# Optimization experiments

Hardware: AMD Instinct MI355X
Metric: run time of the kernel (lower is better)

The kernel has to match this reference:

```python
import jax, jax.numpy as jnp
import numpy as np

B, N, D, H = 8, 2048, 256, 4
HD = D // H


def setup_inputs() -> dict:
    key = jax.random.key(0)
    ks = jax.random.split(key, 12)
    s = 1.0 / np.sqrt(D)
    inp = {
        "node_features": jax.random.normal(ks[0], (B, N, D), dtype=jnp.float32),
        "causal_mask": jnp.tril(jnp.ones((N, N), dtype=jnp.float32)),
        "Wq": jax.random.normal(ks[1], (D, D), dtype=jnp.float32) * s,
        "bq": jnp.zeros((D,), dtype=jnp.float32),
        "Wk": jax.random.normal(ks[2], (D, D), dtype=jnp.float32) * s,
        "bk": jnp.zeros((D,), dtype=jnp.float32),
        "Wv": jax.random.normal(ks[3], (D, D), dtype=jnp.float32) * s,
        "bv": jnp.zeros((D,), dtype=jnp.float32),
        "Wo": jax.random.normal(ks[4], (D, D), dtype=jnp.float32) * s,
        "bo": jnp.zeros((D,), dtype=jnp.float32),
        "Wu": jax.random.normal(ks[5], (2 * D, D), dtype=jnp.float32) * (1.0 / np.sqrt(2 * D)),
        "bu": jnp.zeros((D,), dtype=jnp.float32),
    }
    return inp


def reference(node_features, causal_mask, Wq, bq, Wk, bk, Wv, bv, Wo, bo, Wu, bu):
    # node_features: [B, N, D]; causal_mask: [N, N] (1 = keep, 0 = masked)
    x = node_features
    # project and split heads -> [B, H, N, HD]
    def heads(w, b):
        return (x @ w + b).reshape(B, N, H, HD).transpose(0, 2, 1, 3)
    q, k, v = heads(Wq, bq), heads(Wk, bk), heads(Wv, bv)
    scale = 1.0 / np.sqrt(HD).astype(np.float32)
    scores = jnp.einsum("bhnd,bhmd->bhnm", q, k) * scale  # [B, H, N, N]
    scores = jnp.where(causal_mask > 0, scores, jnp.float32(-1e9))
    attn = jax.nn.softmax(scores, axis=-1)
    ctx = jnp.einsum("bhnm,bhmd->bhnd", attn, v)  # [B, H, N, HD]
    messages = ctx.transpose(0, 2, 1, 3).reshape(B, N, D) @ Wo + bo  # [B, N, D]
    combined = jnp.concatenate([x, messages], axis=-1)  # [B, N, 2D]
    updated = jax.nn.relu(combined @ Wu + bu)  # [B, N, D]  (dropout = identity in eval)
    return updated
```

## Files before the change

### kernel.cpp

```cpp
#include <hip/hip_runtime.h>
#include <math.h>

constexpr int B  = 8;
constexpr int N  = 2048;
constexpr int D  = 256;
constexpr int H  = 4;
constexpr int HD = 64;
constexpr int MTOT = B * N;

typedef __attribute__((ext_vector_type(8))) short  short8;
typedef __attribute__((ext_vector_type(4))) float  floatx4;
typedef unsigned short ushort_t;

#define QSCALE 0.1803368801111204f

__device__ __forceinline__ unsigned short f2bf(float f) {
    unsigned u = __float_as_uint(f);
    u += 0x7fffu + ((u >> 16) & 1u);
    return (unsigned short)(u >> 16);
}

__device__ __forceinline__ unsigned short f2bf_t(float f) {
    return (unsigned short)(__float_as_uint(f) >> 16);
}

__device__ __forceinline__ void gl_lds16(const ushort_t* g, ushort_t* l) {
    __builtin_amdgcn_global_load_lds(
        (const __attribute__((address_space(1))) void*)g,
        (__attribute__((address_space(3))) void*)l, 16, 0, 0);
}

__global__ __launch_bounds__(256) void prep(
    const float* __restrict__ x,
    const float* __restrict__ Wq, const float* __restrict__ Wk,
    const float* __restrict__ Wv, const float* __restrict__ Wo,
    const float* __restrict__ Wu,
    ushort_t* __restrict__ xb,
    ushort_t* __restrict__ wqkvt, ushort_t* __restrict__ wut,
    ushort_t* __restrict__ wbt,   ushort_t* __restrict__ wob)
{
    __shared__ float Ls[64][65];
    const int bx = blockIdx.x;
    const int t  = threadIdx.x;

    if (bx < 2048) {
        int idx = (bx * 256 + t) * 8;
        float4 a = *(const float4*)(x + idx);
        float4 b = *(const float4*)(x + idx + 4);
        ushort_t o[8] = {f2bf(a.x), f2bf(a.y), f2bf(a.z), f2bf(a.w),
                         f2bf(b.x), f2bf(b.y), f2bf(b.z), f2bf(b.w)};
        *(short8*)(xb + idx) = *(const short8*)o;
        return;
    }

    if (bx < 2112) {
        const int e  = bx - 2048;
        const int zz = e >> 4;
        const int kt = (e >> 2) & 3;
        const int nt = e & 3;
        const float* src; ushort_t* dst; int K;
        if      (zz == 0) { src = Wq; dst = wqkvt;          K = 256; }
        else if (zz == 1) { src = Wk; dst = wqkvt + 65536;  K = 256; }
        else if (zz == 2) { src = Wv; dst = wqkvt + 131072; K = 256; }
        else              { src = Wu; dst = wut;            K = 512; }
        #pragma unroll
        for (int i = 0; i < 16; i++) {
            int ee = t + i * 256, r = ee >> 6, c = ee & 63;
            Ls[r][c] = src[(size_t)(kt * 64 + r) * 256 + nt * 64 + c];
        }
        __syncthreads();
        #pragma unroll
        for (int i = 0; i < 16; i++) {
            int ee = t + i * 256, r = ee >> 6, c = ee & 63;
            dst[(size_t)(nt * 64 + r) * K + kt * 64 + c] = f2bf(Ls[c][r]);
        }
        return;
    }

    if (bx < 2128) {
        const int e  = bx - 2112;
        const int kt = e >> 2;
        const int nt = e & 3;
        #pragma unroll
        for (int i = 0; i < 16; i++) {
            int ee = t + i * 256, r = ee >> 6, c = ee & 63;
            Ls[r][c] = Wu[(size_t)(256 + kt * 64 + r) * 256 + nt * 64 + c];
        }
        __syncthreads();
        #pragma unroll
        for (int i = 0; i < 16; i++) {
            int ee = t + i * 256, r = ee >> 6, c = ee & 63;
            wbt[(size_t)(nt * 64 + r) * 256 + kt * 64 + c] = f2bf(Ls[c][r]);
        }
        return;
    }

    {
        int idx = ((bx - 2128) * 256 + t) * 8;
        float4 a = *(const float4*)(Wo + idx);
        float4 b = *(const float4*)(Wo + idx + 4);
        ushort_t o[8] = {f2bf(a.x), f2bf(a.y), f2bf(a.z), f2bf(a.w),
                         f2bf(b.x), f2bf(b.y), f2bf(b.z), f2bf(b.w)};
        *(short8*)(wob + idx) = *(const short8*)o;
    }
}

__global__ __launch_bounds__(256) void qkv_gemm(
    const ushort_t* __restrict__ xb, const ushort_t* __restrict__ wqkvt,
    const ushort_t* __restrict__ wob, const ushort_t* __restrict__ wbt,
    const float* __restrict__ Wu,
    const float* __restrict__ bq, const float* __restrict__ bk,
    const float* __restrict__ bv, const float* __restrict__ bo,
    const float* __restrict__ bu,
    ushort_t* __restrict__ q, ushort_t* __restrict__ kout,
    ushort_t* __restrict__ vt,
    ushort_t* __restrict__ wut, float* __restrict__ b2)
{
    __shared__ ushort_t SH[16896];
    ushort_t* As = SH;
    ushort_t* Bs = SH + 8192;

    const int t = threadIdx.x, w = t >> 6, lane = t & 63;
    const int quad = lane >> 4, l16 = lane & 15;
    const int bx = blockIdx.x;
    const int wr = (w >> 1) * 64, wc = (w & 1) * 64;

    if (blockIdx.y == 128) {
        if (bx < 4) {
            const int row0 = (bx >> 1) * 128;
            const int col0 = (bx & 1) * 128;
            floatx4 acc[4][4] = {};
            for (int k0 = 0; k0 < 256; k0 += 64) {
                __syncthreads();
                #pragma unroll
                for (int i = 0; i < 4; i++) {
                    int e = t + (i << 8);
                    int r = e >> 3, c8 = (e & 7) << 3;
                    gl_lds16(wob + (size_t)(row0 + r) * 256 + k0 + c8, &As[e * 8]);
                    gl_lds16(wbt + (size_t)(col0 + r) * 256 + k0 + c8, &Bs[e * 8]);
                }
                __syncthreads();
                #pragma unroll
                for (int kk = 0; kk < 64; kk += 32) {
                    short8 af[4], bf[4];
                    #pragma unroll
                    for (int i = 0; i < 4; i++)
                        af[i] = *(const short8*)&As[(wr + i * 16 + l16) * 64 + kk + quad * 8];
                    #pragma unroll
                    for (int j = 0; j < 4; j++)
                        bf[j] = *(const short8*)&Bs[(wc + j * 16 + l16) * 64 + kk + quad * 8];
                    #pragma unroll
                    for (int i = 0; i < 4; i++)
                        #pragma unroll
                        for (int j = 0; j < 4; j++)
                            acc[i][j] = __builtin_amdgcn_mfma_f32_16x16x32_bf16(
                                af[i], bf[j], acc[i][j], 0, 0, 0);
                }
            }
            #pragma unroll
            for (int j = 0; j < 4; j++) {
                int cl = wc + j * 16 + l16;
                #pragma unroll
                for (int i = 0; i < 4; i++)
                    #pragma unroll
                    for (int r = 0; r < 4; r++) {
                        int ml = wr + i * 16 + quad * 4 + r;
                        wut[(size_t)(col0 + cl) * 512 + 256 + row0 + ml] =
                            f2bf(acc[i][j][r]);
                    }
            }
        } else if (bx == 4) {
            float s0 = 0.f, s1 = 0.f, s2 = 0.f, s3 = 0.f;
            for (int j = 0; j < 64; j++) {
                s0 = fmaf(bo[j],       Wu[(size_t)(256 + j)       * 256 + t], s0);
                s1 = fmaf(bo[j + 64],  Wu[(size_t)(256 + j + 64)  * 256 + t], s1);
                s2 = fmaf(bo[j + 128], Wu[(size_t)(256 + j + 128) * 256 + t], s2);
                s3 = fmaf(bo[j + 192], Wu[(size_t)(256 + j + 192) * 256 + t], s3);
            }
            b2[t] = bu[t] + ((s0 + s1) + (s2 + s3));
        }
        return;
    }

    const int col0 = bx * 128, row0 = blockIdx.y * 128;

    floatx4 acc[4][4] = {};

    for (int k0 = 0; k0 < 256; k0 += 64) {
        __syncthreads();
        #pragma unroll
        for (int i = 0; i < 4; i++) {
            int e = t + (i << 8);
            int r = e >> 3, c8 = (e & 7) << 3;
            gl_lds16(xb    + (size_t)(row0 + r) * 256 + k0 + c8, &As[e * 8]);
            gl_lds16(wqkvt + (size_t)(col0 + r) * 256 + k0 + c8, &Bs[e * 8]);
        }
        __syncthreads();

        #pragma unroll
        for (int kk = 0; kk < 64; kk += 32) {
            short8 af[4], bf[4];
            #pragma unroll
            for (int i = 0; i < 4; i++)
                af[i] = *(const short8*)&As[(wr + i * 16 + l16) * 64 + kk + quad * 8];
            #pragma unroll
            for (int j = 0; j < 4; j++)
                bf[j] = *(const short8*)&Bs[(wc + j * 16 + l16) * 64 + kk + quad * 8];
            #pragma unroll
            for (int i = 0; i < 4; i++)
                #pragma unroll
                for (int j = 0; j < 4; j++)
                    acc[i][j] = __builtin_amdgcn_mfma_f32_16x16x32_bf16(
                        af[i], bf[j], acc[i][j], 0, 0, 0);
        }
    }

    const int kind = bx >> 1;
    const float* bias = (kind == 0) ? bq : (kind == 1 ? bk : bv);
    const float scl  = (kind == 0) ? QSCALE : 1.0f;
    __syncthreads();
    ushort_t (*Ts)[132] = (ushort_t(*)[132])SH;
    #pragma unroll
    for (int j = 0; j < 4; j++) {
        int cl = wc + j * 16 + l16;
        float bsv = bias[(bx & 1) * 128 + cl];
        #pragma unroll
        for (int i = 0; i < 4; i++) {
            #pragma unroll
            for (int r = 0; r < 4; r++) {
                int ml = wr + i * 16 + quad * 4 + r;
                ushort_t bvv = f2bf((acc[i][j][r] + bsv) * scl);
                if (kind < 2) Ts[ml][cl] = bvv;
                else          Ts[cl][ml] = bvv;
            }
        }
    }
    __syncthreads();

    const int b = row0 >> 11, n0 = row0 & (N - 1);
    #pragma unroll
    for (int i = 0; i < 8; i++) {
        int id = t + (i << 8);
        int rr = id >> 4, c8 = (id & 15) << 3;
        short8 val = *(const short8*)&Ts[rr][c8];
        if (kind < 2) {
            int cg = (bx & 1) * 128 + c8;
            int h = cg >> 6, hd = cg & 63;
            if (kind == 0) {
                *(short8*)&q[(((size_t)(b * H + h)) * N + n0 + rr) * HD + hd] = val;
            } else {
                int hd2 = (((hd >> 3) ^ (rr & 7)) << 3);
                *(short8*)&kout[(((size_t)(b * H + h)) * N + n0 + rr) * HD + hd2] = val;
            }
        } else {
            int cg = (bx & 1) * 128 + rr;
            int h = cg >> 6, hd = cg & 63;
            int u  = id & 15;
            int up = (u & 8) | ((u ^ hd) & 7);
            *(short8*)&vt[(((size_t)(b * H + h)) * HD + hd) * N + n0 + (up << 3)] = val;
        }
    }
}

__global__ __launch_bounds__(512) void attn_mfma(
    const ushort_t* __restrict__ q,
    const ushort_t* __restrict__ k,
    const ushort_t* __restrict__ vt,
    ushort_t* __restrict__ ctxb)
{
    __shared__ ushort_t Ks [128 * 64];
    __shared__ ushort_t Vts[64 * 128];
    __shared__ ushort_t Ps [8][16][36];

    const int t    = threadIdx.x;
    const int w    = t >> 6;
    const int lane = t & 63;
    const int quad = lane >> 4;
    const int l16  = lane & 15;
    const int swz  = l16 & 7;
    const int bh   = blockIdx.x;
    const int b    = bh >> 2, h = bh & 3;
    const int by   = blockIdx.y;
    const int grp  = w >> 2;
    const int qt   = grp ? by : (31 - by);
    const int qbase = qt * 64;
    const int rowb  = qbase + (w & 3) * 16;

    const ushort_t* qp = q  + (size_t)bh * N * HD;
    const ushort_t* kp = k  + (size_t)bh * N * HD;
    const ushort_t* vp = vt + (size_t)bh * HD * N;

    short8 qf0, qf1;
    {
        const ushort_t* qrow = qp + (size_t)(rowb + l16) * HD + quad * 8;
        qf0 = *(const short8*)(qrow);
        qf1 = *(const short8*)(qrow + 32);
    }

    floatx4 acc_o[4] = {};
    float plsum[4] = {};

    const int nkt_self = (qt >> 1) + 1;
    const int nkt_max  = ((31 - by) >> 1) + 1;

    for (int kt = 0; kt < nkt_max; kt++) {
        const int kbase = kt * 128;
        __syncthreads();

        #pragma unroll
        for (int i = 0; i < 2; i++) {
            int e = t + (i << 9);
            gl_lds16(kp + (((size_t)(kbase + (e >> 3))) << 6) + ((e & 7) << 3),
                     &Ks[e * 8]);
            gl_lds16(vp + (size_t)(e >> 4) * N + kbase + ((e & 15) << 3),
                     &Vts[e * 8]);
        }
        __syncthreads();

        if (kt >= nkt_self) continue;

        int rem = rowb + 15 - kbase;
        int nch = (rem < 0) ? 0 : ((rem >> 5) + 1);
        if (nch > 4) nch = 4;

        for (int ch = 0; ch < nch; ch++) {
            #pragma unroll
            for (int c2 = 0; c2 < 2; c2++) {
                const int ct = ch * 2 + c2;
                const int krow = (ct * 16 + l16) * 64;
                short8 kf0 = *(const short8*)&Ks[krow + ((quad ^ swz) << 3)];
                short8 kf1 = *(const short8*)&Ks[krow + (((4 + quad) ^ swz) << 3)];
                floatx4 z = {0.0f, 0.0f, 0.0f, 0.0f};
                floatx4 s = __builtin_amdgcn_mfma_f32_16x16x32_bf16(qf0, kf0, z, 0, 0, 0);
                s         = __builtin_amdgcn_mfma_f32_16x16x32_bf16(qf1, kf1, s, 0, 0, 0);
                const bool partial = (kbase + ct * 16 + 15) > rowb;
                if (partial) {
                    const int keyg = kbase + ct * 16 + l16;
                    #pragma unroll
                    for (int r = 0; r < 4; r++) {
                        float sv = s[r];
                        if (keyg > rowb + quad * 4 + r) sv = -3.0e38f;
                        float pv = __builtin_amdgcn_exp2f(sv);
                        plsum[r] += pv;
                        Ps[w][quad * 4 + r][c2 * 16 + l16] = f2bf_t(pv);
                    }
                } else {
                    #pragma unroll
                    for (int r = 0; r < 4; r++) {
                        float pv = __builtin_amdgcn_exp2f(s[r]);
                        plsum[r] += pv;
                        Ps[w][quad * 4 + r][c2 * 16 + l16] = f2bf_t(pv);
                    }
                }
            }
            short8 pf = *(const short8*)&Ps[w][l16][quad * 8];
            const int uu = ch * 4 + quad;
            const int up = (uu & 8) | ((uu ^ l16) & 7);
            #pragma unroll
            for (int nt = 0; nt < 4; nt++) {
                short8 vf = *(const short8*)&Vts[(nt * 16 + l16) * 128 + (up << 3)];
                acc_o[nt] = __builtin_amdgcn_mfma_f32_16x16x32_bf16(pf, vf, acc_o[nt], 0, 0, 0);
            }
        }
    }

    #pragma unroll
    for (int r = 0; r < 4; r++) {
        float l = plsum[r];
        l += __shfl_xor(l, 1);
        l += __shfl_xor(l, 2);
        l += __shfl_xor(l, 4);
        l += __shfl_xor(l, 8);
        float inv = 1.0f / l;
        int   n   = rowb + quad * 4 + r;
        #pragma unroll
        for (int nt = 0; nt < 4; nt++) {
            ctxb[((size_t)(b * N + n)) * D + h * HD + nt * 16 + l16] =
                f2bf(acc_o[nt][r] * inv);
        }
    }
}

__global__ __launch_bounds__(256) void tail2(
    const ushort_t* __restrict__ xb, const ushort_t* __restrict__ ctxb,
    const ushort_t* __restrict__ wut, const float* __restrict__ b2,
    float* __restrict__ out)
{
    __shared__ ushort_t As[64 * 64];
    __shared__ ushort_t Bs[128 * 64];

    const int t = threadIdx.x, w = t >> 6, lane = t & 63;
    const int quad = lane >> 4, l16 = lane & 15;
    const int col0 = blockIdx.x * 128, row0 = blockIdx.y * 64;
    const int wr = (w >> 1) * 32, wc = (w & 1) * 64;

    floatx4 acc[2][4] = {};

    for (int k0 = 0; k0 < 512; k0 += 64) {
        const ushort_t* Ab = (k0 < 256) ? xb : ctxb;
        const int ka = k0 & 255;
        __syncthreads();
        #pragma unroll
        for (int i = 0; i < 2; i++) {
            int e = t + (i << 8);
            int r = e >> 3, c8 = (e & 7) << 3;
            gl_lds16(Ab + (size_t)(row0 + r) * 256 + ka + c8, &As[e * 8]);
        }
        #pragma unroll
        for (int i = 0; i < 4; i++) {
            int e = t + (i << 8);
            int r = e >> 3, c8 = (e & 7) << 3;
            gl_lds16(wut + (size_t)(col0 + r) * 512 + k0 + c8, &Bs[e * 8]);
        }
        __syncthreads();

        #pragma unroll
        for (int kk = 0; kk < 64; kk += 32) {
            short8 af[2], bf[4];
            #pragma unroll
            for (int i = 0; i < 2; i++)
                af[i] = *(const short8*)&As[(wr + i * 16 + l16) * 64 + kk + quad * 8];
            #pragma unroll
            for (int j = 0; j < 4; j++)
                bf[j] = *(const short8*)&Bs[(wc + j * 16 + l16) * 64 + kk + quad * 8];
            #pragma unroll
            for (int i = 0; i < 2; i++)
                #pragma unroll
                for (int j = 0; j < 4; j++)
                    acc[i][j] = __builtin_amdgcn_mfma_f32_16x16x32_bf16(
                        af[i], bf[j], acc[i][j], 0, 0, 0);
        }
    }

    #pragma unroll
    for (int j = 0; j < 4; j++) {
        int col = col0 + wc + j * 16 + l16;
        float bsv = b2[col];
        #pragma unroll
        for (int i = 0; i < 2; i++) {
            #pragma unroll
            for (int r = 0; r < 4; r++) {
                int m = row0 + wr + i * 16 + quad * 4 + r;
                out[(size_t)m * 256 + col] = fmaxf(acc[i][j][r] + bsv, 0.0f);
            }
        }
    }
}

extern "C" void kernel_launch(void* const* d_in, const int* in_sizes, int n_in,
                              void* d_out, int out_size, void* d_ws, size_t ws_size,
                              hipStream_t stream)
{
    const float* x  = (const float*)d_in[0];
    const float* Wq = (const float*)d_in[2];
    const float* bq = (const float*)d_in[3];
    const float* Wk = (const float*)d_in[4];
    const float* bk = (const float*)d_in[5];
    const float* Wv = (const float*)d_in[6];
    const float* bv = (const float*)d_in[7];
    const float* Wo = (const float*)d_in[8];
    const float* bo = (const float*)d_in[9];
    const float* Wu = (const float*)d_in[10];
    const float* bu = (const float*)d_in[11];
    float* out = (float*)d_out;

    const size_t SZ = (size_t)MTOT * D;
    ushort_t* xb    = (ushort_t*)d_ws;
    ushort_t* qb    = xb    + SZ;
    ushort_t* kb    = qb    + SZ;
    ushort_t* vbt   = kb    + SZ;
    ushort_t* ctxb  = vbt   + SZ;
    ushort_t* wqkvt = ctxb  + SZ;
    ushort_t* wut   = wqkvt + 196608;
    ushort_t* wbt   = wut   + 131072;
    ushort_t* wob   = wbt   + 65536;
    float*    b2    = (float*)(wob + 65536);

    prep<<<2160, 256, 0, stream>>>(x, Wq, Wk, Wv, Wo, Wu,
                                   xb, wqkvt, wut, wbt, wob);

    qkv_gemm<<<dim3(6, 129), 256, 0, stream>>>(
        xb, wqkvt, wob, wbt, Wu, bq, bk, bv, bo, bu,
        qb, kb, vbt, wut, b2);

    attn_mfma<<<dim3(32, 16), 512, 0, stream>>>(qb, kb, vbt, ctxb);

    tail2<<<dim3(2, 256), 256, 0, stream>>>(xb, ctxb, wut, b2, out);
}
```

Before: 170.7 us.

## Double-buffer K/V tiles in LDS and raise wave priority around MFMAs

```diff
diff --git a/kernel.cpp b/kernel.cpp
--- a/kernel.cpp
+++ b/kernel.cpp
@@ -268,8 +268,8 @@
     const ushort_t* __restrict__ vt,
     ushort_t* __restrict__ ctxb)
 {
-    __shared__ ushort_t Ks [128 * 64];
-    __shared__ ushort_t Vts[64 * 128];
+    __shared__ ushort_t Ks [2][128 * 64];
+    __shared__ ushort_t Vts[2][64 * 128];
     __shared__ ushort_t Ps [8][16][36];
 
     const int t    = threadIdx.x;
@@ -303,65 +303,86 @@
     const int nkt_self = (qt >> 1) + 1;
     const int nkt_max  = ((31 - by) >> 1) + 1;
 
+    #pragma unroll
+    for (int i = 0; i < 2; i++) {
+        int e = t + (i << 9);
+        gl_lds16(kp + (((size_t)(e >> 3)) << 6) + ((e & 7) << 3),
+                 &Ks[0][e * 8]);
+        gl_lds16(vp + (size_t)(e >> 4) * N + ((e & 15) << 3),
+                 &Vts[0][e * 8]);
+    }
+    __syncthreads();
+
     for (int kt = 0; kt < nkt_max; kt++) {
         const int kbase = kt * 128;
-        __syncthreads();
-
-        #pragma unroll
-        for (int i = 0; i < 2; i++) {
-            int e = t + (i << 9);
-            gl_lds16(kp + (((size_t)(kbase + (e >> 3))) << 6) + ((e & 7) << 3),
-                     &Ks[e * 8]);
-            gl_lds16(vp + (size_t)(e >> 4) * N + kbase + ((e & 15) << 3),
-                     &Vts[e * 8]);
-        }
-        __syncthreads();
-
-        if (kt >= nkt_self) continue;
-
-        int rem = rowb + 15 - kbase;
-        int nch = (rem < 0) ? 0 : ((rem >> 5) + 1);
-        if (nch > 4) nch = 4;
-
-        for (int ch = 0; ch < nch; ch++) {
-            #pragma unroll
-            for (int c2 = 0; c2 < 2; c2++) {
-                const int ct = ch * 2 + c2;
-                const int krow = (ct * 16 + l16) * 64;
-                short8 kf0 = *(const short8*)&Ks[krow + ((quad ^ swz) << 3)];
-                short8 kf1 = *(const short8*)&Ks[krow + (((4 + quad) ^ swz) << 3)];
-                floatx4 z = {0.0f, 0.0f, 0.0f, 0.0f};
-                floatx4 s = __builtin_amdgcn_mfma_f32_16x16x32_bf16(qf0, kf0, z, 0, 0, 0);
-                s         = __builtin_amdgcn_mfma_f32_16x16x32_bf16(qf1, kf1, s, 0, 0, 0);
-                const bool partial = (kbase + ct * 16 + 15) > rowb;
-                if (partial) {
-                    const int keyg = kbase + ct * 16 + l16;
-                    #pragma unroll
-                    for (int r = 0; r < 4; r++) {
-                        float sv = s[r];
-                        if (keyg > rowb + quad * 4 + r) sv = -3.0e38f;
-                        float pv = __builtin_amdgcn_exp2f(sv);
-                        plsum[r] += pv;
-                        Ps[w][quad * 4 + r][c2 * 16 + l16] = f2bf_t(pv);
-                    }
-                } else {
-                    #pragma unroll
-                    for (int r = 0; r < 4; r++) {
-                        float pv = __builtin_amdgcn_exp2f(s[r]);
-                        plsum[r] += pv;
-                        Ps[w][quad * 4 + r][c2 * 16 + l16] = f2bf_t(pv);
+        const int cur   = kt & 1;
+
+        if (kt + 1 < nkt_max) {
+            const int kb2 = kbase + 128;
+            #pragma unroll
+            for (int i = 0; i < 2; i++) {
+                int e = t + (i << 9);
+                gl_lds16(kp + (((size_t)(kb2 + (e >> 3))) << 6) + ((e & 7) << 3),
+                         &Ks[cur ^ 1][e * 8]);
+                gl_lds16(vp + (size_t)(e >> 4) * N + kb2 + ((e & 15) << 3),
+                         &Vts[cur ^ 1][e * 8]);
+            }
+        }
+
+        if (kt < nkt_self) {
+            const ushort_t* Ksc  = Ks[cur];
+            const ushort_t* Vtsc = Vts[cur];
+
+            int rem = rowb + 15 - kbase;
+            int nch = (rem < 0) ? 0 : ((rem >> 5) + 1);
+            if (nch > 4) nch = 4;
+
+            for (int ch = 0; ch < nch; ch++) {
+                #pragma unroll
+                for (int c2 = 0; c2 < 2; c2++) {
+                    const int ct = ch * 2 + c2;
+                    const int krow = (ct * 16 + l16) * 64;
+                    short8 kf0 = *(const short8*)&Ksc[krow + ((quad ^ swz) << 3)];
+                    short8 kf1 = *(const short8*)&Ksc[krow + (((4 + quad) ^ swz) << 3)];
+                    floatx4 z = {0.0f, 0.0f, 0.0f, 0.0f};
+                    __builtin_amdgcn_s_setprio(1);
+                    floatx4 s = __builtin_amdgcn_mfma_f32_16x16x32_bf16(qf0, kf0, z, 0, 0, 0);
+                    s         = __builtin_amdgcn_mfma_f32_16x16x32_bf16(qf1, kf1, s, 0, 0, 0);
+                    __builtin_amdgcn_s_setprio(0);
+                    const bool partial = (kbase + ct * 16 + 15) > rowb;
+                    if (partial) {
+                        const int keyg = kbase + ct * 16 + l16;
+                        #pragma unroll
+                        for (int r = 0; r < 4; r++) {
+                            float sv = s[r];
+                            if (keyg > rowb + quad * 4 + r) sv = -3.0e38f;
+                            float pv = __builtin_amdgcn_exp2f(sv);
+                            plsum[r] += pv;
+                            Ps[w][quad * 4 + r][c2 * 16 + l16] = f2bf_t(pv);
+                        }
+                    } else {
+                        #pragma unroll
+                        for (int r = 0; r < 4; r++) {
+                            float pv = __builtin_amdgcn_exp2f(s[r]);
+                            plsum[r] += pv;
+                            Ps[w][quad * 4 + r][c2 * 16 + l16] = f2bf_t(pv);
+                        }
                     }
                 }
-            }
-            short8 pf = *(const short8*)&Ps[w][l16][quad * 8];
-            const int uu = ch * 4 + quad;
-            const int up = (uu & 8) | ((uu ^ l16) & 7);
-            #pragma unroll
-            for (int nt = 0; nt < 4; nt++) {
-                short8 vf = *(const short8*)&Vts[(nt * 16 + l16) * 128 + (up << 3)];
-                acc_o[nt] = __builtin_amdgcn_mfma_f32_16x16x32_bf16(pf, vf, acc_o[nt], 0, 0, 0);
-            }
-        }
+                short8 pf = *(const short8*)&Ps[w][l16][quad * 8];
+                const int uu = ch * 4 + quad;
+                const int up = (uu & 8) | ((uu ^ l16) & 7);
+                __builtin_amdgcn_s_setprio(1);
+                #pragma unroll
+                for (int nt = 0; nt < 4; nt++) {
+                    short8 vf = *(const short8*)&Vtsc[(nt * 16 + l16) * 128 + (up << 3)];
+                    acc_o[nt] = __builtin_amdgcn_mfma_f32_16x16x32_bf16(pf, vf, acc_o[nt], 0, 0, 0);
+                }
+                __builtin_amdgcn_s_setprio(0);
+            }
+        }
+
+        __syncthreads();
     }
 
     #pragma unroll
```

Measured after the change: 167.5 us. About the same (-1.9%).
